# Kernel tuning notes

Hardware: AMD Instinct MI355X
Metric: run time of the kernel (lower is better)

The kernel has to match this reference:

```python
import jax, jax.numpy as jnp
import numpy as np

IMAGE_W = 640
IMAGE_H = 640
SCALE = jnp.array([0.1, 0.1, 0.2, 0.2], dtype=jnp.float32)
TOP_N = 1000
MIN_SCORE = 0.05
NMS_THR = 0.5
MAX_DET = 100


def setup_inputs() -> dict:
    key = jax.random.key(0)
    kc, kr, k1, k2 = jax.random.split(key, 4)
    B, A, C = 8, 120000, 80
    cls_heads = jax.random.uniform(kc, (B, A, C), dtype=jnp.float32)  # sigmoid-like scores
    reg_heads = jax.random.normal(kr, (B, A, 4), dtype=jnp.float32)
    # valid anchors: centers inside image, wh in [16, 256]
    ctr = jax.random.uniform(k1, (B, A, 2), minval=0.0, maxval=640.0, dtype=jnp.float32)
    wh = jax.random.uniform(k2, (B, A, 2), minval=16.0, maxval=256.0, dtype=jnp.float32)
    batch_anchors = jnp.concatenate([ctr - 0.5 * wh, ctr + 0.5 * wh], axis=-1)
    return {"cls_heads": cls_heads, "reg_heads": reg_heads, "batch_anchors": batch_anchors}


def _decode(reg, anchors):
    # reg: [N,4] (tx,ty,tw,th), anchors: [N,4] (x1,y1,x2,y2)
    awh = anchors[:, 2:] - anchors[:, :2]
    actr = anchors[:, :2] + 0.5 * awh
    reg = reg * SCALE
    pwh = jnp.exp(reg[:, 2:]) * awh
    pctr = reg[:, :2] * awh + actr
    boxes = jnp.concatenate([pctr - 0.5 * pwh, pctr + 0.5 * pwh], axis=1)
    boxes = jnp.trunc(boxes)  # mimics torch .int() truncation
    boxes = jnp.stack([
        jnp.maximum(boxes[:, 0], 0.0),
        jnp.maximum(boxes[:, 1], 0.0),
        jnp.minimum(boxes[:, 2], float(IMAGE_W - 1)),
        jnp.minimum(boxes[:, 3], float(IMAGE_H - 1)),
    ], axis=1)
    return boxes


def _nms_image(scores, classes, boxes):
    # scores sorted descending (from top_k); class-agnostic greedy NMS.
    N = scores.shape[0]
    valid = scores > MIN_SCORE
    area = (boxes[:, 2] - boxes[:, 0]) * (boxes[:, 3] - boxes[:, 1])
    lt = jnp.maximum(boxes[:, None, :2], boxes[None, :, :2])
    rb = jnp.minimum(boxes[:, None, 2:], boxes[None, :, 2:])
    inter = jnp.prod(jnp.clip(rb - lt, 0.0, None), axis=-1)  # [N,N]
    iou = inter / (area[:, None] + area[None, :] - inter)
    idx = jnp.arange(N)

    def body(i, keep):
        supp = (iou[i] > NMS_THR) & (idx > i) & keep[i]
        return keep & ~supp

    keep = jax.lax.fori_loop(0, N, body, valid)
    order = jnp.argsort(~keep, stable=True)  # kept first, score order preserved
    take = order[:MAX_DET]
    n_keep = jnp.sum(keep)
    slot = jnp.arange(MAX_DET) < n_keep
    out_s = jnp.where(slot, scores[take], -1.0)
    out_c = jnp.where(slot, classes[take].astype(jnp.float32), -1.0)
    out_b = jnp.where(slot[:, None], boxes[take], -1.0)
    return out_s, out_c, out_b


def reference(cls_heads, reg_heads, batch_anchors):
    # per-anchor best class
    scores0 = jnp.max(cls_heads, axis=2)          # [B,A]
    classes0 = jnp.argmax(cls_heads, axis=2)      # [B,A]
    top_scores, top_idx = jax.lax.top_k(scores0, TOP_N)  # sorted descending
    top_classes = jnp.take_along_axis(classes0, top_idx, axis=1)
    top_reg = jnp.take_along_axis(reg_heads, top_idx[..., None], axis=1)
    top_anchors = jnp.take_along_axis(batch_anchors, top_idx[..., None], axis=1)

    def per_image(s, c, r, a):
        boxes = _decode(r, a)
        return _nms_image(s, c, boxes)

    batch_scores, batch_classes, batch_bboxes = jax.vmap(per_image)(
        top_scores, top_classes, top_reg, top_anchors)
    return batch_scores, batch_classes, batch_bboxes
```

## Files before the change

kernel.cpp:

```cpp
#include <hip/hip_runtime.h>
#include <math.h>

#define AN 120000
#define NB 8
#define NC 80
#define TOPN 1000
#define MAXDET 100
#define CAND_CAP 2048
#define CAND_T 0.99985f

typedef unsigned long long u64;
typedef unsigned int u32;

__device__ __forceinline__ float opaquef(float x) { asm volatile("" : "+v"(x)); return x; }

__global__ __launch_bounds__(256) void score_kernel(const float* __restrict__ cls,
                                                    u64* __restrict__ keys,
                                                    int* __restrict__ cls_out,
                                                    u64* __restrict__ cand,
                                                    u32* __restrict__ cand_cnt) {
    __shared__ float buf[4][32 * 81];
    const int tid = threadIdx.x;
    const int wave = tid >> 6, lane = tid & 63;
    const long long blockbase = (long long)blockIdx.x * 256;

    for (int h = 0; h < 2; ++h) {
        const long long abase = blockbase + wave * 64 + h * 32;
        const float4* src = (const float4*)(cls + abase * NC);
        float* Bf = buf[wave];
#pragma unroll
        for (int it = 0; it < 10; ++it) {
            int f = lane + it * 64;
            float4 v = src[f];
            int anch = f / 20, pos = (f % 20) * 4;
            float* dst = Bf + anch * 81 + pos;
            dst[0] = v.x; dst[1] = v.y; dst[2] = v.z; dst[3] = v.w;
        }
        __syncthreads();
        int anch = lane >> 1, half = lane & 1;
        const float* row = Bf + anch * 81 + half * 40;
        float best = -1.0f; int bi = 0;
#pragma unroll
        for (int i = 0; i < 40; ++i) {
            float v = row[i];
            if (v > best) { best = v; bi = i; }
        }
        bi += half * 40;
        float ov = __shfl_xor(best, 1);
        int   oi = __shfl_xor(bi, 1);
        if (ov > best || (ov == best && oi < bi)) { best = ov; bi = oi; }
        if (half == 0) {
            long long aglob = abase + anch;
            int a = (int)(aglob % AN);
            u64 key = ((u64)__float_as_uint(best) << 17) | (u64)(131071 - a);
            keys[aglob]    = key;
            cls_out[aglob] = bi;
            if (best >= CAND_T) {
                int im = (int)(aglob / AN);
                u32 p = atomicAdd(&cand_cnt[im], 1u);
                if (p < CAND_CAP) cand[(size_t)im * CAND_CAP + p] = key;
            }
        }
        __syncthreads();
    }
}

__global__ __launch_bounds__(1024) void select_kernel(const u64* __restrict__ keys,
                                                      const u64* __restrict__ cand,
                                                      const u32* __restrict__ cand_cnt,
                                                      u64* __restrict__ topk) {
    const int img = blockIdx.x;
    const int tid = threadIdx.x;

    __shared__ u64 stopk[CAND_CAP];
    __shared__ u32 hist[256];
    __shared__ u32 sscan[256];
    __shared__ u32 s_need, s_digit, s_cnt;
    __shared__ u64 s_prefix;

    const u32 cnt = cand_cnt[img];
    if (cnt >= (u32)TOPN && cnt <= (u32)CAND_CAP) {
        const u64* c = cand + (size_t)img * CAND_CAP;
        for (int i = tid; i < CAND_CAP; i += 1024)
            stopk[i] = (i < (int)cnt) ? ~c[i] : ~0ull;
        __syncthreads();
        for (int kk = 2; kk <= CAND_CAP; kk <<= 1) {
            for (int j = kk >> 1; j > 0; j >>= 1) {
                for (int i = tid; i < CAND_CAP; i += 1024) {
                    int ixj = i ^ j;
                    if (ixj > i) {
                        u64 a = stopk[i], b = stopk[ixj];
                        bool asc = ((i & kk) == 0);
                        if ((a > b) == asc) { stopk[i] = b; stopk[ixj] = a; }
                    }
                }
                __syncthreads();
            }
        }
        topk[img * 1024 + tid] = ~stopk[tid];
        return;
    }

    const u64* k = keys + (size_t)img * AN;

    if (tid == 0) { s_need = TOPN; s_prefix = 0; s_cnt = 0; }
    if (tid < 1024) stopk[tid] = ~0ull;
    __syncthreads();

    for (int lvl = 0; lvl < 6; ++lvl) {
        const int shift = 40 - 8 * lvl;
        if (tid < 256) hist[tid] = 0;
        __syncthreads();
        const u64 P = s_prefix;
        const u32 need = s_need;
        for (int i = tid; i < AN; i += 1024) {
            u64 K = k[i];
            if ((K >> (shift + 8)) == P)
                atomicAdd(&hist[(u32)((K >> shift) & 255)], 1u);
        }
        __syncthreads();
        if (tid < 256) sscan[tid] = hist[tid];
        __syncthreads();
        for (int off = 1; off < 256; off <<= 1) {
            u32 v = 0;
            if (tid < 256 && tid + off < 256) v = sscan[tid + off];
            __syncthreads();
            if (tid < 256) sscan[tid] += v;
            __syncthreads();
        }
        if (tid < 256) {
            u32 above = (tid == 255) ? 0u : sscan[tid + 1];
            if (sscan[tid] >= need && above < need) {
                s_digit = (u32)tid;
                s_need = need - above;
            }
        }
        __syncthreads();
        if (tid == 0) s_prefix = (s_prefix << 8) | (u64)s_digit;
        __syncthreads();
    }

    const u64 T = s_prefix;
    for (int i = tid; i < AN; i += 1024) {
        u64 K = k[i];
        if (K >= T) {
            u32 pos = atomicAdd(&s_cnt, 1u);
            if (pos < 1024) stopk[pos] = ~K;
        }
    }
    __syncthreads();

    for (int kk = 2; kk <= 1024; kk <<= 1) {
        for (int j = kk >> 1; j > 0; j >>= 1) {
            int ixj = tid ^ j;
            if (ixj > tid) {
                u64 a = stopk[tid], b = stopk[ixj];
                bool asc = ((tid & kk) == 0);
                if ((a > b) == asc) { stopk[tid] = b; stopk[ixj] = a; }
            }
            __syncthreads();
        }
    }
    topk[img * 1024 + tid] = ~stopk[tid];
}

__global__ __launch_bounds__(256) void decode_kernel(const u64* __restrict__ topk,
                                                     const int* __restrict__ clsin,
                                                     const float* __restrict__ reg,
                                                     const float* __restrict__ anch,
                                                     float* __restrict__ tsc,
                                                     int* __restrict__ tcl,
                                                     float* __restrict__ tbox) {
    int t = blockIdx.x * 256 + threadIdx.x;
    if (t >= NB * 1024) return;
    int img = t >> 10, j = t & 1023;
    if (j >= TOPN) return;

    u64 K = topk[t];
    u32 sb = (u32)(K >> 17);
    int idx = 131071 - (int)(K & 0x1FFFF);
    float score = __uint_as_float(sb);
    size_t gi = (size_t)img * AN + idx;

    float4 r = ((const float4*)reg)[gi];
    float4 a = ((const float4*)anch)[gi];

    float aw = a.z - a.x, ah = a.w - a.y;
    float acx = a.x + 0.5f * aw, acy = a.y + 0.5f * ah;
    float rx = opaquef(r.x * 0.1f), ry = opaquef(r.y * 0.1f);
    float rw = opaquef(r.z * 0.2f), rh = opaquef(r.w * 0.2f);
    float pw = opaquef((float)exp((double)rw) * aw);
    float ph = opaquef((float)exp((double)rh) * ah);
    float pcx = opaquef(rx * aw) + acx;
    float pcy = opaquef(ry * ah) + acy;
    float x1 = truncf(pcx - 0.5f * pw);
    float y1 = truncf(pcy - 0.5f * ph);
    float x2 = truncf(pcx + 0.5f * pw);
    float y2 = truncf(pcy + 0.5f * ph);
    x1 = fmaxf(x1, 0.0f); y1 = fmaxf(y1, 0.0f);
    x2 = fminf(x2, 639.0f); y2 = fminf(y2, 639.0f);

    tsc[t] = score;
    tcl[t] = clsin[gi];
    ((float4*)tbox)[t] = make_float4(x1, y1, x2, y2);
}

__global__ __launch_bounds__(256) void mask_kernel(const float* __restrict__ tbox,
                                                   u64* __restrict__ masks) {
    __shared__ float4 sb[1000];
    __shared__ float  sarea[1000];
    const int img = blockIdx.x / 250;
    const int grp = blockIdx.x % 250;
    const int tid = threadIdx.x;

    for (int t = tid; t < 1000; t += 256) {
        float4 b = ((const float4*)tbox)[img * 1024 + t];
        sb[t] = b;
        sarea[t] = (b.z - b.x) * (b.w - b.y);
    }
    __syncthreads();

    const int wave = tid >> 6, lane = tid & 63;
    const int i = grp * 4 + wave;
    float4 bi = sb[i];
    float  ai = sarea[i];
#pragma unroll
    for (int w = 0; w < 16; ++w) {
        int j = w * 64 + lane;
        bool p = false;
        if (j < 1000 && j > i) {
            float4 bj = sb[j];
            float ltx = fmaxf(bi.x, bj.x), lty = fmaxf(bi.y, bj.y);
            float rbx = fminf(bi.z, bj.z), rby = fminf(bi.w, bj.w);
            float dx = fmaxf(rbx - ltx, 0.0f), dy = fmaxf(rby - lty, 0.0f);
            float inter = dx * dy;
            float uni = ai + sarea[j] - inter;
            p = (inter / uni) > 0.5f;
        }
        u64 m = __ballot(p);
        if (lane == 0) masks[((size_t)img * 1000 + i) * 16 + w] = m;
    }
}

__global__ __launch_bounds__(64) void scan_kernel(const u64* __restrict__ masks,
                                                  const float* __restrict__ tsc,
                                                  const int* __restrict__ tcl,
                                                  const float* __restrict__ tbox,
                                                  float* __restrict__ out) {
    const int img = blockIdx.x;
    const int lane = threadIdx.x;
    __shared__ int keeplist[MAXDET];
    __shared__ float ssc[TOPN];

    for (int i = lane; i < TOPN; i += 64) ssc[i] = tsc[img * 1024 + i];
    __syncthreads();

    u64 remv = 0;
    int kept = 0;
    for (int i = 0; i < TOPN; ++i) {
        int word = i >> 6, bit = i & 63;
        u64 rw = __shfl(remv, word);
        bool removed = (rw >> bit) & 1ull;
        float sc = ssc[i];
        if (sc > 0.05f && !removed) {
            if (lane == 0) keeplist[kept] = i;
            kept++;
            if (kept >= MAXDET) break;
            if (lane < 16) remv |= masks[((size_t)img * 1000 + i) * 16 + lane];
        }
    }
    __syncthreads();

    const int n_keep = kept;
    for (int s = lane; s < MAXDET; s += 64) {
        int o = img * MAXDET + s;
        if (s < n_keep) {
            int i = keeplist[s];
            out[o] = ssc[i];
            out[NB * MAXDET + o] = (float)tcl[img * 1024 + i];
            ((float4*)(out + 2 * NB * MAXDET))[o] = ((const float4*)tbox)[img * 1024 + i];
        } else {
            out[o] = -1.0f;
            out[NB * MAXDET + o] = -1.0f;
            ((float4*)(out + 2 * NB * MAXDET))[o] = make_float4(-1.0f, -1.0f, -1.0f, -1.0f);
        }
    }
}

extern "C" void kernel_launch(void* const* d_in, const int* in_sizes, int n_in,
                              void* d_out, int out_size, void* d_ws, size_t ws_size,
                              hipStream_t stream) {
    const float* cls  = (const float*)d_in[0];
    const float* reg  = (const float*)d_in[1];
    const float* anch = (const float*)d_in[2];
    float* out = (float*)d_out;

    u64* keys   = (u64*)d_ws;
    u64* topk   = keys + (size_t)NB * AN;
    u64* masks  = topk + NB * 1024;
    u64* cand   = masks + (size_t)NB * 1000 * 16;
    int* clsmax = (int*)(cand + (size_t)NB * CAND_CAP);
    float* tbox = (float*)(clsmax + (size_t)NB * AN);
    float* tsc  = tbox + NB * 1024 * 4;
    int*   tcl  = (int*)(tsc + NB * 1024);
    u32*   ccnt = (u32*)(tcl + NB * 1024);

    hipMemsetAsync(ccnt, 0, NB * sizeof(u32), stream);
    hipLaunchKernelGGL(score_kernel,  dim3(3750), dim3(256),  0, stream, cls, keys, clsmax, cand, ccnt);
    hipLaunchKernelGGL(select_kernel, dim3(NB),   dim3(1024), 0, stream, keys, cand, ccnt, topk);
    hipLaunchKernelGGL(decode_kernel, dim3(32),   dim3(256),  0, stream, topk, clsmax, reg, anch, tsc, tcl, tbox);
    hipLaunchKernelGGL(mask_kernel,   dim3(2000), dim3(256),  0, stream, tbox, masks);
    hipLaunchKernelGGL(scan_kernel,   dim3(NB),   dim3(64),   0, stream, masks, tsc, tcl, tbox, out);
}
```

Measured before the change: 544.6 us.

## Fuse top-k select, decode, and NMS into a single per-image kernel

Merges the selection, box decode, IoU mask and greedy scan kernels into one block per image that keeps boxes, scores and classes in shared memory. NMS now computes IoU rows on demand only for kept boxes, using per-lane register-cached candidate boxes, instead of building a full pairwise mask matrix in global memory. This removes three kernel launches and intermediate global traffic. In exchange, the IoU work that was spread over many blocks now runs serially in a single wave per image.

```diff
diff --git a/kernel.cpp b/kernel.cpp
--- a/kernel.cpp
+++ b/kernel.cpp
@@ -65,16 +65,24 @@
     }
 }
 
-__global__ __launch_bounds__(1024) void select_kernel(const u64* __restrict__ keys,
-                                                      const u64* __restrict__ cand,
-                                                      const u32* __restrict__ cand_cnt,
-                                                      u64* __restrict__ topk) {
+__global__ __launch_bounds__(1024) void topk_nms_kernel(const u64* __restrict__ keys,
+                                                        const u64* __restrict__ cand,
+                                                        const u32* __restrict__ cand_cnt,
+                                                        const int* __restrict__ clsin,
+                                                        const float* __restrict__ reg,
+                                                        const float* __restrict__ anch,
+                                                        float* __restrict__ out) {
     const int img = blockIdx.x;
     const int tid = threadIdx.x;
 
     __shared__ u64 stopk[CAND_CAP];
+    __shared__ float4 sbox[TOPN];
     __shared__ u32 hist[256];
     __shared__ u32 sscan[256];
+    __shared__ float ssc[TOPN];
+    __shared__ int   scl[TOPN];
+    __shared__ int keeplist[MAXDET];
+    __shared__ int s_nkeep;
     __shared__ u32 s_need, s_digit, s_cnt;
     __shared__ u64 s_prefix;
 
@@ -97,192 +105,148 @@
                 __syncthreads();
             }
         }
-        topk[img * 1024 + tid] = ~stopk[tid];
-        return;
-    }
-
-    const u64* k = keys + (size_t)img * AN;
-
-    if (tid == 0) { s_need = TOPN; s_prefix = 0; s_cnt = 0; }
-    if (tid < 1024) stopk[tid] = ~0ull;
-    __syncthreads();
-
-    for (int lvl = 0; lvl < 6; ++lvl) {
-        const int shift = 40 - 8 * lvl;
-        if (tid < 256) hist[tid] = 0;
-        __syncthreads();
-        const u64 P = s_prefix;
-        const u32 need = s_need;
+    } else {
+        const u64* k = keys + (size_t)img * AN;
+        if (tid == 0) { s_need = TOPN; s_prefix = 0; s_cnt = 0; }
+        stopk[tid] = ~0ull;
+        __syncthreads();
+
+        for (int lvl = 0; lvl < 6; ++lvl) {
+            const int shift = 40 - 8 * lvl;
+            if (tid < 256) hist[tid] = 0;
+            __syncthreads();
+            const u64 P = s_prefix;
+            const u32 need = s_need;
+            for (int i = tid; i < AN; i += 1024) {
+                u64 K = k[i];
+                if ((K >> (shift + 8)) == P)
+                    atomicAdd(&hist[(u32)((K >> shift) & 255)], 1u);
+            }
+            __syncthreads();
+            if (tid < 256) sscan[tid] = hist[tid];
+            __syncthreads();
+            for (int off = 1; off < 256; off <<= 1) {
+                u32 v = 0;
+                if (tid < 256 && tid + off < 256) v = sscan[tid + off];
+                __syncthreads();
+                if (tid < 256) sscan[tid] += v;
+                __syncthreads();
+            }
+            if (tid < 256) {
+                u32 above = (tid == 255) ? 0u : sscan[tid + 1];
+                if (sscan[tid] >= need && above < need) {
+                    s_digit = (u32)tid;
+                    s_need = need - above;
+                }
+            }
+            __syncthreads();
+            if (tid == 0) s_prefix = (s_prefix << 8) | (u64)s_digit;
+            __syncthreads();
+        }
+
+        const u64 T = s_prefix;
         for (int i = tid; i < AN; i += 1024) {
             u64 K = k[i];
-            if ((K >> (shift + 8)) == P)
-                atomicAdd(&hist[(u32)((K >> shift) & 255)], 1u);
-        }
-        __syncthreads();
-        if (tid < 256) sscan[tid] = hist[tid];
-        __syncthreads();
-        for (int off = 1; off < 256; off <<= 1) {
-            u32 v = 0;
-            if (tid < 256 && tid + off < 256) v = sscan[tid + off];
-            __syncthreads();
-            if (tid < 256) sscan[tid] += v;
-            __syncthreads();
-        }
-        if (tid < 256) {
-            u32 above = (tid == 255) ? 0u : sscan[tid + 1];
-            if (sscan[tid] >= need && above < need) {
-                s_digit = (u32)tid;
-                s_need = need - above;
-            }
-        }
-        __syncthreads();
-        if (tid == 0) s_prefix = (s_prefix << 8) | (u64)s_digit;
-        __syncthreads();
-    }
-
-    const u64 T = s_prefix;
-    for (int i = tid; i < AN; i += 1024) {
-        u64 K = k[i];
-        if (K >= T) {
-            u32 pos = atomicAdd(&s_cnt, 1u);
-            if (pos < 1024) stopk[pos] = ~K;
-        }
+            if (K >= T) {
+                u32 pos = atomicAdd(&s_cnt, 1u);
+                if (pos < 1024) stopk[pos] = ~K;
+            }
+        }
+        __syncthreads();
+        for (int kk = 2; kk <= 1024; kk <<= 1) {
+            for (int j = kk >> 1; j > 0; j >>= 1) {
+                int ixj = tid ^ j;
+                if (ixj > tid) {
+                    u64 a = stopk[tid], b = stopk[ixj];
+                    bool asc = ((tid & kk) == 0);
+                    if ((a > b) == asc) { stopk[tid] = b; stopk[ixj] = a; }
+                }
+                __syncthreads();
+            }
+        }
+    }
+
+    if (tid < TOPN) {
+        u64 K = ~stopk[tid];
+        u32 sb = (u32)(K >> 17);
+        int idx = 131071 - (int)(K & 0x1FFFF);
+        float score = __uint_as_float(sb);
+        size_t gi = (size_t)img * AN + idx;
+
+        float4 r = ((const float4*)reg)[gi];
+        float4 a = ((const float4*)anch)[gi];
+
+        float aw = a.z - a.x, ah = a.w - a.y;
+        float acx = a.x + 0.5f * aw, acy = a.y + 0.5f * ah;
+        float rx = opaquef(r.x * 0.1f), ry = opaquef(r.y * 0.1f);
+        float rw = opaquef(r.z * 0.2f), rh = opaquef(r.w * 0.2f);
+        float pw = opaquef((float)exp((double)rw) * aw);
+        float ph = opaquef((float)exp((double)rh) * ah);
+        float pcx = opaquef(rx * aw) + acx;
+        float pcy = opaquef(ry * ah) + acy;
+        float x1 = truncf(pcx - 0.5f * pw);
+        float y1 = truncf(pcy - 0.5f * ph);
+        float x2 = truncf(pcx + 0.5f * pw);
+        float y2 = truncf(pcy + 0.5f * ph);
+        x1 = fmaxf(x1, 0.0f); y1 = fmaxf(y1, 0.0f);
+        x2 = fminf(x2, 639.0f); y2 = fminf(y2, 639.0f);
+
+        sbox[tid] = make_float4(x1, y1, x2, y2);
+        ssc[tid]  = score;
+        scl[tid]  = clsin[gi];
     }
     __syncthreads();
 
-    for (int kk = 2; kk <= 1024; kk <<= 1) {
-        for (int j = kk >> 1; j > 0; j >>= 1) {
-            int ixj = tid ^ j;
-            if (ixj > tid) {
-                u64 a = stopk[tid], b = stopk[ixj];
-                bool asc = ((tid & kk) == 0);
-                if ((a > b) == asc) { stopk[tid] = b; stopk[ixj] = a; }
-            }
-            __syncthreads();
-        }
-    }
-    topk[img * 1024 + tid] = ~stopk[tid];
-}
-
-__global__ __launch_bounds__(256) void decode_kernel(const u64* __restrict__ topk,
-                                                     const int* __restrict__ clsin,
-                                                     const float* __restrict__ reg,
-                                                     const float* __restrict__ anch,
-                                                     float* __restrict__ tsc,
-                                                     int* __restrict__ tcl,
-                                                     float* __restrict__ tbox) {
-    int t = blockIdx.x * 256 + threadIdx.x;
-    if (t >= NB * 1024) return;
-    int img = t >> 10, j = t & 1023;
-    if (j >= TOPN) return;
-
-    u64 K = topk[t];
-    u32 sb = (u32)(K >> 17);
-    int idx = 131071 - (int)(K & 0x1FFFF);
-    float score = __uint_as_float(sb);
-    size_t gi = (size_t)img * AN + idx;
-
-    float4 r = ((const float4*)reg)[gi];
-    float4 a = ((const float4*)anch)[gi];
-
-    float aw = a.z - a.x, ah = a.w - a.y;
-    float acx = a.x + 0.5f * aw, acy = a.y + 0.5f * ah;
-    float rx = opaquef(r.x * 0.1f), ry = opaquef(r.y * 0.1f);
-    float rw = opaquef(r.z * 0.2f), rh = opaquef(r.w * 0.2f);
-    float pw = opaquef((float)exp((double)rw) * aw);
-    float ph = opaquef((float)exp((double)rh) * ah);
-    float pcx = opaquef(rx * aw) + acx;
-    float pcy = opaquef(ry * ah) + acy;
-    float x1 = truncf(pcx - 0.5f * pw);
-    float y1 = truncf(pcy - 0.5f * ph);
-    float x2 = truncf(pcx + 0.5f * pw);
-    float y2 = truncf(pcy + 0.5f * ph);
-    x1 = fmaxf(x1, 0.0f); y1 = fmaxf(y1, 0.0f);
-    x2 = fminf(x2, 639.0f); y2 = fminf(y2, 639.0f);
-
-    tsc[t] = score;
-    tcl[t] = clsin[gi];
-    ((float4*)tbox)[t] = make_float4(x1, y1, x2, y2);
-}
-
-__global__ __launch_bounds__(256) void mask_kernel(const float* __restrict__ tbox,
-                                                   u64* __restrict__ masks) {
-    __shared__ float4 sb[1000];
-    __shared__ float  sarea[1000];
-    const int img = blockIdx.x / 250;
-    const int grp = blockIdx.x % 250;
-    const int tid = threadIdx.x;
-
-    for (int t = tid; t < 1000; t += 256) {
-        float4 b = ((const float4*)tbox)[img * 1024 + t];
-        sb[t] = b;
-        sarea[t] = (b.z - b.x) * (b.w - b.y);
+    if (tid < 64) {
+        const int lane = tid;
+        float4 bj[16]; float aj[16];
+#pragma unroll
+        for (int w = 0; w < 16; ++w) {
+            int j = w * 64 + lane;
+            float4 b = (j < TOPN) ? sbox[j] : make_float4(0.f, 0.f, 0.f, 0.f);
+            bj[w] = b;
+            aj[w] = (b.z - b.x) * (b.w - b.y);
+        }
+        u32 pmask = 0;
+        int kept = 0;
+        for (int i = 0; i < TOPN; ++i) {
+            u32 pm = __shfl(pmask, i & 63);
+            bool removed = (pm >> (i >> 6)) & 1u;
+            float sc = ssc[i];
+            float4 bi = sbox[i];
+            if (sc > 0.05f && !removed) {
+                if (lane == 0) keeplist[kept] = i;
+                kept++;
+                if (kept >= MAXDET) break;
+                float ai = (bi.z - bi.x) * (bi.w - bi.y);
+#pragma unroll
+                for (int w = 0; w < 16; ++w) {
+                    int j = w * 64 + lane;
+                    float ltx = fmaxf(bi.x, bj[w].x), lty = fmaxf(bi.y, bj[w].y);
+                    float rbx = fminf(bi.z, bj[w].z), rby = fminf(bi.w, bj[w].w);
+                    float dx = fmaxf(rbx - ltx, 0.0f), dy = fmaxf(rby - lty, 0.0f);
+                    float inter = dx * dy;
+                    float uni = ai + aj[w] - inter;
+                    bool p = (j < TOPN) && (j > i) && ((inter / uni) > 0.5f);
+                    pmask |= p ? (1u << w) : 0u;
+                }
+            }
+        }
+        if (lane == 0) s_nkeep = kept;
     }
     __syncthreads();
 
-    const int wave = tid >> 6, lane = tid & 63;
-    const int i = grp * 4 + wave;
-    float4 bi = sb[i];
-    float  ai = sarea[i];
-#pragma unroll
-    for (int w = 0; w < 16; ++w) {
-        int j = w * 64 + lane;
-        bool p = false;
-        if (j < 1000 && j > i) {
-            float4 bj = sb[j];
-            float ltx = fmaxf(bi.x, bj.x), lty = fmaxf(bi.y, bj.y);
-            float rbx = fminf(bi.z, bj.z), rby = fminf(bi.w, bj.w);
-            float dx = fmaxf(rbx - ltx, 0.0f), dy = fmaxf(rby - lty, 0.0f);
-            float inter = dx * dy;
-            float uni = ai + sarea[j] - inter;
-            p = (inter / uni) > 0.5f;
-        }
-        u64 m = __ballot(p);
-        if (lane == 0) masks[((size_t)img * 1000 + i) * 16 + w] = m;
-    }
-}
-
-__global__ __launch_bounds__(64) void scan_kernel(const u64* __restrict__ masks,
-                                                  const float* __restrict__ tsc,
-                                                  const int* __restrict__ tcl,
-                                                  const float* __restrict__ tbox,
-                                                  float* __restrict__ out) {
-    const int img = blockIdx.x;
-    const int lane = threadIdx.x;
-    __shared__ int keeplist[MAXDET];
-    __shared__ float ssc[TOPN];
-
-    for (int i = lane; i < TOPN; i += 64) ssc[i] = tsc[img * 1024 + i];
-    __syncthreads();
-
-    u64 remv = 0;
-    int kept = 0;
-    for (int i = 0; i < TOPN; ++i) {
-        int word = i >> 6, bit = i & 63;
-        u64 rw = __shfl(remv, word);
-        bool removed = (rw >> bit) & 1ull;
-        float sc = ssc[i];
-        if (sc > 0.05f && !removed) {
-            if (lane == 0) keeplist[kept] = i;
-            kept++;
-            if (kept >= MAXDET) break;
-            if (lane < 16) remv |= masks[((size_t)img * 1000 + i) * 16 + lane];
-        }
-    }
-    __syncthreads();
-
-    const int n_keep = kept;
-    for (int s = lane; s < MAXDET; s += 64) {
-        int o = img * MAXDET + s;
-        if (s < n_keep) {
-            int i = keeplist[s];
+    if (tid < MAXDET) {
+        int o = img * MAXDET + tid;
+        if (tid < s_nkeep) {
+            int i = keeplist[tid];
             out[o] = ssc[i];
-            out[NB * MAXDET + o] = (float)tcl[img * 1024 + i];
-            ((float4*)(out + 2 * NB * MAXDET))[o] = ((const float4*)tbox)[img * 1024 + i];
+            out[NB * MAXDET + o] = (float)scl[i];
+            ((float4*)(out + 2 * NB * MAXDET))[o] = sbox[i];
         } else {
             out[o] = -1.0f;
             out[NB * MAXDET + o] = -1.0f;
-            ((float4*)(out + 2 * NB * MAXDET))[o] = make_float4(-1.0f, -1.0f, -1.0f, -1.0f);
+            ((float4*)(out + 2 * NB * MAXDET))[o] = make_float4(-1.f, -1.f, -1.f, -1.f);
         }
     }
 }
@@ -296,19 +260,11 @@
     float* out = (float*)d_out;
 
     u64* keys   = (u64*)d_ws;
-    u64* topk   = keys + (size_t)NB * AN;
-    u64* masks  = topk + NB * 1024;
-    u64* cand   = masks + (size_t)NB * 1000 * 16;
+    u64* cand   = keys + (size_t)NB * AN;
     int* clsmax = (int*)(cand + (size_t)NB * CAND_CAP);
-    float* tbox = (float*)(clsmax + (size_t)NB * AN);
-    float* tsc  = tbox + NB * 1024 * 4;
-    int*   tcl  = (int*)(tsc + NB * 1024);
-    u32*   ccnt = (u32*)(tcl + NB * 1024);
+    u32* ccnt   = (u32*)(clsmax + (size_t)NB * AN);
 
     hipMemsetAsync(ccnt, 0, NB * sizeof(u32), stream);
-    hipLaunchKernelGGL(score_kernel,  dim3(3750), dim3(256),  0, stream, cls, keys, clsmax, cand, ccnt);
-    hipLaunchKernelGGL(select_kernel, dim3(NB),   dim3(1024), 0, stream, keys, cand, ccnt, topk);
-    hipLaunchKernelGGL(decode_kernel, dim3(32),   dim3(256),  0, stream, topk, clsmax, reg, anch, tsc, tcl, tbox);
-    hipLaunchKernelGGL(mask_kernel,   dim3(2000), dim3(256),  0, stream, tbox, masks);
-    hipLaunchKernelGGL(scan_kernel,   dim3(NB),   dim3(64),   0, stream, masks, tsc, tcl, tbox, out);
+    hipLaunchKernelGGL(score_kernel,    dim3(3750), dim3(256),  0, stream, cls, keys, clsmax, cand, ccnt);
+    hipLaunchKernelGGL(topk_nms_kernel, dim3(NB),   dim3(1024), 0, stream, keys, cand, ccnt, clsmax, reg, anch, out);
 }
```

Measured after the change: 626.5 us. +15.0%, slower.

## Skip suppressed candidates in NMS scan using per-word alive bitmask

Applied to the files above, without the earlier changes.

The greedy NMS scan no longer steps through all 1000 candidates one at a time. For each 64-candidate word it builds an alive bitmask from a ballot on the scores and the accumulated removal mask, then jumps between survivors with count-trailing-zeros. Intra-word suppression comes from a transposed mask copy that the mask kernel now also writes. This trades serial per-candidate iterations for an extra scattered write per mask word and a dependent global load per kept box.

```diff
diff --git a/kernel.cpp b/kernel.cpp
--- a/kernel.cpp
+++ b/kernel.cpp
@@ -104,7 +104,7 @@
     const u64* k = keys + (size_t)img * AN;
 
     if (tid == 0) { s_need = TOPN; s_prefix = 0; s_cnt = 0; }
-    if (tid < 1024) stopk[tid] = ~0ull;
+    stopk[tid] = ~0ull;
     __syncthreads();
 
     for (int lvl = 0; lvl < 6; ++lvl) {
@@ -206,7 +206,8 @@
 }
 
 __global__ __launch_bounds__(256) void mask_kernel(const float* __restrict__ tbox,
-                                                   u64* __restrict__ masks) {
+                                                   u64* __restrict__ masks,
+                                                   u64* __restrict__ masks_t) {
     __shared__ float4 sb[1000];
     __shared__ float  sarea[1000];
     const int img = blockIdx.x / 250;
@@ -238,11 +239,15 @@
             p = (inter / uni) > 0.5f;
         }
         u64 m = __ballot(p);
-        if (lane == 0) masks[((size_t)img * 1000 + i) * 16 + w] = m;
+        if (lane == 0) {
+            masks[((size_t)img * 1000 + i) * 16 + w] = m;
+            masks_t[((size_t)img * 16 + w) * 1000 + i] = m;
+        }
     }
 }
 
 __global__ __launch_bounds__(64) void scan_kernel(const u64* __restrict__ masks,
+                                                  const u64* __restrict__ masks_t,
                                                   const float* __restrict__ tsc,
                                                   const int* __restrict__ tcl,
                                                   const float* __restrict__ tbox,
@@ -250,23 +255,26 @@
     const int img = blockIdx.x;
     const int lane = threadIdx.x;
     __shared__ int keeplist[MAXDET];
-    __shared__ float ssc[TOPN];
-
-    for (int i = lane; i < TOPN; i += 64) ssc[i] = tsc[img * 1024 + i];
+    __shared__ float ssc[1024];
+
+    for (int i = lane; i < 1024; i += 64)
+        ssc[i] = (i < TOPN) ? tsc[img * 1024 + i] : -1.0f;
     __syncthreads();
 
     u64 remv = 0;
     int kept = 0;
-    for (int i = 0; i < TOPN; ++i) {
-        int word = i >> 6, bit = i & 63;
-        u64 rw = __shfl(remv, word);
-        bool removed = (rw >> bit) & 1ull;
-        float sc = ssc[i];
-        if (sc > 0.05f && !removed) {
+    for (int w = 0; w < 16 && kept < MAXDET; ++w) {
+        u64 alive = __ballot(ssc[w * 64 + lane] > 0.05f) & ~__shfl(remv, w);
+        while (alive) {
+            int b = __builtin_ctzll(alive);
+            int i = w * 64 + b;
             if (lane == 0) keeplist[kept] = i;
             kept++;
             if (kept >= MAXDET) break;
+            u64 mw = masks_t[((size_t)img * 16 + w) * 1000 + i];
             if (lane < 16) remv |= masks[((size_t)img * 1000 + i) * 16 + lane];
+            alive &= ~mw;
+            alive &= (b < 63) ? (~0ull << (b + 1)) : 0ull;
         }
     }
     __syncthreads();
@@ -295,20 +303,21 @@
     const float* anch = (const float*)d_in[2];
     float* out = (float*)d_out;
 
-    u64* keys   = (u64*)d_ws;
-    u64* topk   = keys + (size_t)NB * AN;
-    u64* masks  = topk + NB * 1024;
-    u64* cand   = masks + (size_t)NB * 1000 * 16;
-    int* clsmax = (int*)(cand + (size_t)NB * CAND_CAP);
-    float* tbox = (float*)(clsmax + (size_t)NB * AN);
-    float* tsc  = tbox + NB * 1024 * 4;
-    int*   tcl  = (int*)(tsc + NB * 1024);
-    u32*   ccnt = (u32*)(tcl + NB * 1024);
+    u64* keys    = (u64*)d_ws;
+    u64* topk    = keys + (size_t)NB * AN;
+    u64* masks   = topk + NB * 1024;
+    u64* masks_t = masks + (size_t)NB * 1000 * 16;
+    u64* cand    = masks_t + (size_t)NB * 16 * 1000;
+    int* clsmax  = (int*)(cand + (size_t)NB * CAND_CAP);
+    float* tbox  = (float*)(clsmax + (size_t)NB * AN);
+    float* tsc   = tbox + NB * 1024 * 4;
+    int*   tcl   = (int*)(tsc + NB * 1024);
+    u32*   ccnt  = (u32*)(tcl + NB * 1024);
 
     hipMemsetAsync(ccnt, 0, NB * sizeof(u32), stream);
     hipLaunchKernelGGL(score_kernel,  dim3(3750), dim3(256),  0, stream, cls, keys, clsmax, cand, ccnt);
     hipLaunchKernelGGL(select_kernel, dim3(NB),   dim3(1024), 0, stream, keys, cand, ccnt, topk);
     hipLaunchKernelGGL(decode_kernel, dim3(32),   dim3(256),  0, stream, topk, clsmax, reg, anch, tsc, tcl, tbox);
-    hipLaunchKernelGGL(mask_kernel,   dim3(2000), dim3(256),  0, stream, tbox, masks);
-    hipLaunchKernelGGL(scan_kernel,   dim3(NB),   dim3(64),   0, stream, masks, tsc, tcl, tbox, out);
-}
+    hipLaunchKernelGGL(mask_kernel,   dim3(2000), dim3(256),  0, stream, tbox, masks, masks_t);
+    hipLaunchKernelGGL(scan_kernel,   dim3(NB),   dim3(64),   0, stream, masks, masks_t, tsc, tcl, tbox, out);
+}
```

Result: no change. 547.7 us (+0.6%).
